# Kernel optimization log

Hardware: AMD Instinct MI355X
Metric: run time of the kernel (lower is better)

Reference implementation:

```python
import jax, jax.numpy as jnp
import numpy as np


def _sage_conv(x, src, dst, num_nodes, Wl, Wr, b):
    # PyG SAGEConv (aggr='mean'): out = lin_l(mean_{j in N(i)} x_j) + lin_r(x_i)
    msgs = x[src]                                            # [E, d] gather
    agg = jax.ops.segment_sum(msgs, dst, num_segments=num_nodes)   # [N, d]
    deg = jax.ops.segment_sum(jnp.ones((src.shape[0],), x.dtype), dst,
                              num_segments=num_nodes)        # [N]
    mean = agg / jnp.clip(deg, 1.0)[:, None]                 # isolated nodes -> 0
    return mean @ Wl.T + b + x @ Wr.T


def setup_inputs() -> dict:
    key = jax.random.key(0)
    ks = jax.random.split(key, 12)
    N, E, d = 100000, 1600000, 64
    sizes = [64, 64, 32]
    x = jax.random.normal(ks[0], (N, d), dtype=jnp.float32)
    edge_index = jax.random.randint(ks[1], (2, E), 0, N, dtype=jnp.int64)
    edge_weight = jax.random.uniform(ks[2], (E,), dtype=jnp.float32)
    inp = {"x": x, "edge_index": edge_index, "edge_weight": edge_weight}
    cur = d
    for i, out_dim in enumerate(sizes):
        s = 1.0 / np.sqrt(cur)
        inp[f"Wl{i}"] = jax.random.uniform(ks[3 + 3 * i], (out_dim, cur), jnp.float32, -s, s)
        inp[f"Wr{i}"] = jax.random.uniform(ks[4 + 3 * i], (out_dim, cur), jnp.float32, -s, s)
        inp[f"b{i}"] = jax.random.uniform(ks[5 + 3 * i], (out_dim,), jnp.float32, -s, s)
        cur = out_dim
    return inp


def reference(x, edge_index, edge_weight, Wl0, Wr0, b0, Wl1, Wr1, b1, Wl2, Wr2, b2):
    # edge_weight is intentionally ignored (GraphSAGE ignores edge weights).
    N = x.shape[0]
    src, dst = edge_index[0], edge_index[1]
    h = jax.nn.relu(_sage_conv(x, src, dst, N, Wl0, Wr0, b0))
    h = jax.nn.relu(_sage_conv(h, src, dst, N, Wl1, Wr1, b1))
    h = _sage_conv(h, src, dst, N, Wl2, Wr2, b2)
    return h
```

## Files before the change

kernel.cpp:

```cpp
#include <hip/hip_runtime.h>
#include <hip/hip_fp16.h>


#define MAXB 512
#define NBLK 512
#define NSLICE 8

typedef _Float16 f16;
typedef __attribute__((ext_vector_type(4))) _Float16 f16x4;
typedef __attribute__((ext_vector_type(8))) _Float16 f16x8;
typedef __attribute__((ext_vector_type(4))) float f32x4;

__global__ __launch_bounds__(256) void hist_k(const int* __restrict__ dst, int E,
                                              int nb, int* __restrict__ ghist) {
    __shared__ int h[MAXB];
    for (int i = threadIdx.x; i < nb; i += 256) h[i] = 0;
    __syncthreads();
    int chunk = (E + NBLK - 1) / NBLK;
    int e0 = blockIdx.x * chunk, e1 = min(e0 + chunk, E);
    for (int e = e0 + threadIdx.x; e < e1; e += 256) atomicAdd(&h[dst[e] >> 8], 1);
    __syncthreads();
    for (int i = threadIdx.x; i < nb; i += 256) ghist[blockIdx.x * MAXB + i] = h[i];
}

__global__ __launch_bounds__(512) void col_scan_k(int* __restrict__ ghist,
                                                  int* __restrict__ colsum) {
    int bucket = blockIdx.x;
    int t = threadIdx.x;
    __shared__ int s[NBLK];
    int v = ghist[t * MAXB + bucket];
    s[t] = v;
    __syncthreads();
    for (int off = 1; off < NBLK; off <<= 1) {
        int x = (t >= off) ? s[t - off] : 0;
        __syncthreads();
        s[t] += x;
        __syncthreads();
    }
    ghist[t * MAXB + bucket] = s[t] - v;
    if (t == NBLK - 1) colsum[bucket] = s[NBLK - 1];
}

__global__ __launch_bounds__(512) void bucket_scan_k(const int* __restrict__ colsum,
                                                     int* __restrict__ bbase, int nb) {
    __shared__ int s[512];
    int t = threadIdx.x;
    int v = (t < nb) ? colsum[t] : 0;
    s[t] = v;
    __syncthreads();
    for (int off = 1; off < 512; off <<= 1) {
        int x = (t >= off) ? s[t - off] : 0;
        __syncthreads();
        s[t] += x;
        __syncthreads();
    }
    if (t < nb) bbase[t] = s[t] - v;
}

__global__ __launch_bounds__(256) void partition_k(const int* __restrict__ src,
                                                   const int* __restrict__ dst,
                                                   const int* __restrict__ ghist,
                                                   const int* __restrict__ bbase,
                                                   unsigned* __restrict__ pairs,
                                                   int E, int nb) {
    __shared__ int cur[MAXB];
    for (int i = threadIdx.x; i < nb; i += 256)
        cur[i] = bbase[i] + ghist[blockIdx.x * MAXB + i];
    __syncthreads();
    int chunk = (E + NBLK - 1) / NBLK;
    int e0 = blockIdx.x * chunk, e1 = min(e0 + chunk, E);
    for (int e = e0 + threadIdx.x; e < e1; e += 256) {
        int d = dst[e];
        int b = d >> 8;
        int pos = atomicAdd(&cur[b], 1);
        pairs[pos] = ((unsigned)(d & 255) << 24) | (unsigned)src[e];
    }
}

__global__ __launch_bounds__(256) void bucket_fill2_k(const unsigned* __restrict__ pairs,
                                                      const int* __restrict__ bbase,
                                                      const int* __restrict__ colsum,
                                                      int* __restrict__ rowptr,
                                                      int* __restrict__ adj,
                                                      int N, int E) {
    int b = blockIdx.x, t = threadIdx.x;
    int node0 = b << 8;
    int nloc = min(256, N - node0);
    int e0 = bbase[b];
    int e1 = e0 + colsum[b];
    __shared__ int cnt[256 * NSLICE];
    __shared__ int base[256 * NSLICE];
    __shared__ int bs[256];
#pragma unroll
    for (int k = 0; k < NSLICE; k++) cnt[t * NSLICE + k] = 0;
    __syncthreads();
    for (int e = e0 + t; e < e1; e += 256) {
        unsigned p = pairs[e];
        int local = p >> 24;
        int s = (int)((p & 0xFFFFFFu) >> 14);
        atomicAdd(&cnt[local * NSLICE + s], 1);
    }
    __syncthreads();
    int lv[NSLICE];
    int lsum = 0;
#pragma unroll
    for (int k = 0; k < NSLICE; k++) { lv[k] = cnt[t * NSLICE + k]; lsum += lv[k]; }
    bs[t] = lsum;
    __syncthreads();
    for (int off = 1; off < 256; off <<= 1) {
        int x = (t >= off) ? bs[t - off] : 0;
        __syncthreads();
        bs[t] += x;
        __syncthreads();
    }
    int run = e0 + bs[t] - lsum;
    if (t < nloc) rowptr[node0 + t] = run;
    if (b == 0 && t == 0) rowptr[N] = E;
#pragma unroll
    for (int k = 0; k < NSLICE; k++) { base[t * NSLICE + k] = run; run += lv[k]; }
#pragma unroll
    for (int k = 0; k < NSLICE; k++) cnt[t * NSLICE + k] = 0;
    __syncthreads();
    for (int e = e0 + t; e < e1; e += 256) {
        unsigned p = pairs[e];
        int local = p >> 24;
        int srcv = (int)(p & 0xFFFFFFu);
        int key = local * NSLICE + (srcv >> 14);
        int pos = base[key] + atomicAdd(&cnt[key], 1);
        adj[pos] = srcv;
    }
}


__device__ inline f16x8 cvt2h(float4 a, float4 b) {
    f16x8 o;
    o[0] = (_Float16)a.x; o[1] = (_Float16)a.y; o[2] = (_Float16)a.z; o[3] = (_Float16)a.w;
    o[4] = (_Float16)b.x; o[5] = (_Float16)b.y; o[6] = (_Float16)b.z; o[7] = (_Float16)b.w;
    return o;
}

template <int DOUT, bool AFP32, bool ZF16>
__global__ __launch_bounds__(256) void gemm_mfma_k(const void* __restrict__ A,
                                                   const float* __restrict__ Wl,
                                                   const float* __restrict__ Wr,
                                                   const float* __restrict__ bias,
                                                   __half* __restrict__ Yp,
                                                   void* __restrict__ Zp, int N) {
    constexpr int DOUT2 = 2 * DOUT;
    constexpr int NCT = DOUT2 / 16;
    constexpr int WST = 72;
    __shared__ f16 wlds[DOUT2 * WST];
    int t = threadIdx.x;

    for (int i = t; i < DOUT2 * 16; i += 256) {
        int col = i >> 4, j4 = i & 15;
        const float* wsrc = (col < DOUT) ? (Wl + (size_t)col * 64)
                                         : (Wr + (size_t)(col - DOUT) * 64);
        float4 w = *reinterpret_cast<const float4*>(wsrc + j4 * 4);
        f16x4 o;
        o[0] = (_Float16)w.x; o[1] = (_Float16)w.y;
        o[2] = (_Float16)w.z; o[3] = (_Float16)w.w;
        *reinterpret_cast<f16x4*>(&wlds[col * WST + j4 * 4]) = o;
    }
    __syncthreads();

    int lane = t & 63, wv = t >> 6;
    int r16 = lane & 15;
    int kg = lane >> 4;

    f16x8 bf[NCT][2];
#pragma unroll
    for (int ct = 0; ct < NCT; ct++)
#pragma unroll
        for (int kt = 0; kt < 2; kt++)
            bf[ct][kt] = *reinterpret_cast<const f16x8*>(
                &wlds[(ct * 16 + r16) * WST + kt * 32 + kg * 8]);

    float4 bias4[NCT / 2];
#pragma unroll
    for (int ct = NCT / 2; ct < NCT; ct++)
        bias4[ct - NCT / 2] =
            *reinterpret_cast<const float4*>(bias + ct * 16 + kg * 4 - DOUT);

    int rbase = blockIdx.x * 256 + wv * 64;

#pragma unroll
    for (int rt = 0; rt < 4; rt++) {
        int row0 = rbase + rt * 16;
        int arow = row0 + r16;
        bool valid = arow < N;
        int ar = valid ? arow : (N - 1);

        f16x8 af[2];
        if (AFP32) {
            const float* Af = reinterpret_cast<const float*>(A) + (size_t)ar * 64;
#pragma unroll
            for (int kt = 0; kt < 2; kt++) {
                float4 u = *reinterpret_cast<const float4*>(Af + kt * 32 + kg * 8);
                float4 v = *reinterpret_cast<const float4*>(Af + kt * 32 + kg * 8 + 4);
                af[kt] = cvt2h(u, v);
            }
        } else {
            const f16* Ah = reinterpret_cast<const f16*>(A) + (size_t)ar * 64;
            af[0] = *reinterpret_cast<const f16x8*>(Ah + kg * 8);
            af[1] = *reinterpret_cast<const f16x8*>(Ah + 32 + kg * 8);
        }

        f32x4 acc[NCT];
#pragma unroll
        for (int ct = 0; ct < NCT; ct++) acc[ct] = (f32x4){0.f, 0.f, 0.f, 0.f};
#pragma unroll
        for (int kt = 0; kt < 2; kt++)
#pragma unroll
            for (int ct = 0; ct < NCT; ct++)
                acc[ct] = __builtin_amdgcn_mfma_f32_16x16x32_f16(
                    bf[ct][kt], af[kt], acc[ct], 0, 0, 0);

        if (valid) {
#pragma unroll
            for (int ct = 0; ct < NCT; ct++) {
                int c0 = ct * 16 + kg * 4;
                if (c0 < DOUT) {
                    f16x4 o;
                    o[0] = (_Float16)acc[ct][0]; o[1] = (_Float16)acc[ct][1];
                    o[2] = (_Float16)acc[ct][2]; o[3] = (_Float16)acc[ct][3];
                    *reinterpret_cast<f16x4*>(
                        reinterpret_cast<f16*>(Yp) + (size_t)arow * DOUT + c0) = o;
                } else {
                    float4 bv = bias4[ct - NCT / 2];
                    if (ZF16) {
                        f16x4 z;
                        z[0] = (_Float16)(acc[ct][0] + bv.x);
                        z[1] = (_Float16)(acc[ct][1] + bv.y);
                        z[2] = (_Float16)(acc[ct][2] + bv.z);
                        z[3] = (_Float16)(acc[ct][3] + bv.w);
                        *reinterpret_cast<f16x4*>(
                            reinterpret_cast<f16*>(Zp) + (size_t)arow * DOUT + (c0 - DOUT)) = z;
                    } else {
                        float4 z;
                        z.x = acc[ct][0] + bv.x; z.y = acc[ct][1] + bv.y;
                        z.z = acc[ct][2] + bv.z; z.w = acc[ct][3] + bv.w;
                        *reinterpret_cast<float4*>(
                            reinterpret_cast<float*>(Zp) + (size_t)arow * DOUT + (c0 - DOUT)) = z;
                    }
                }
            }
        }
    }
}


template <int DOUT, bool RELU, bool OUTF16>
__global__ __launch_bounds__(256) void aggregate_k(const int* __restrict__ rp,
                                                   const int* __restrict__ adj,
                                                   const __half* __restrict__ Yh,
                                                   const __half* __restrict__ Zh,
                                                   __half* __restrict__ Ho,
                                                   float* __restrict__ Hf, int N) {
    constexpr int FPR = DOUT / 8;
    constexpr int NPW = 64 / FPR;
    int wave = threadIdx.x >> 6;
    int lane = threadIdx.x & 63;
    int g = lane / FPR;
    int d8 = lane % FPR;
    int node = (blockIdx.x * 4 + wave) * NPW + g;
    if (node >= N) return;
    int s0 = rp[node], s1 = rp[node + 1];
    const float4* Y4 = reinterpret_cast<const float4*>(Yh);
    float acc[8];
#pragma unroll
    for (int k = 0; k < 8; k++) acc[k] = 0.f;

    int e = s0;
    for (; e + 4 <= s1; e += 4) {
        int a0 = adj[e], a1 = adj[e + 1], a2 = adj[e + 2], a3 = adj[e + 3];
        float4 r0 = Y4[(unsigned)a0 * FPR + d8];
        float4 r1 = Y4[(unsigned)a1 * FPR + d8];
        float4 r2 = Y4[(unsigned)a2 * FPR + d8];
        float4 r3 = Y4[(unsigned)a3 * FPR + d8];
        const __half2* h0 = reinterpret_cast<const __half2*>(&r0);
        const __half2* h1 = reinterpret_cast<const __half2*>(&r1);
        const __half2* h2 = reinterpret_cast<const __half2*>(&r2);
        const __half2* h3 = reinterpret_cast<const __half2*>(&r3);
#pragma unroll
        for (int k = 0; k < 4; k++) {
            float2 f0 = __half22float2(h0[k]);
            float2 f1 = __half22float2(h1[k]);
            float2 f2 = __half22float2(h2[k]);
            float2 f3 = __half22float2(h3[k]);
            acc[2 * k]     += (f0.x + f1.x) + (f2.x + f3.x);
            acc[2 * k + 1] += (f0.y + f1.y) + (f2.y + f3.y);
        }
    }
    for (; e < s1; e++) {
        float4 r0 = Y4[(unsigned)adj[e] * FPR + d8];
        const __half2* h0 = reinterpret_cast<const __half2*>(&r0);
#pragma unroll
        for (int k = 0; k < 4; k++) {
            float2 f0 = __half22float2(h0[k]);
            acc[2 * k] += f0.x;
            acc[2 * k + 1] += f0.y;
        }
    }
    int deg = s1 - s0;
    float inv = (deg > 0) ? 1.f / (float)deg : 0.f;

    if constexpr (OUTF16) {
        f16x8 zf = *reinterpret_cast<const f16x8*>(
            reinterpret_cast<const f16*>(Zh) + (size_t)node * DOUT + d8 * 8);
        f16x8 o;
#pragma unroll
        for (int k = 0; k < 8; k++) {
            float tv = (float)zf[k] + acc[k] * inv;
            if (RELU) tv = fmaxf(tv, 0.f);
            o[k] = (_Float16)tv;
        }
        *reinterpret_cast<f16x8*>(reinterpret_cast<f16*>(Ho) + (size_t)node * DOUT + d8 * 8) = o;
    } else {
        float4* H4 = reinterpret_cast<float4*>(Hf);
        size_t hb = (size_t)node * (DOUT / 4) + d8 * 2;
        float4 v0 = H4[hb], v1 = H4[hb + 1];
        v0.x += acc[0] * inv; v0.y += acc[1] * inv;
        v0.z += acc[2] * inv; v0.w += acc[3] * inv;
        v1.x += acc[4] * inv; v1.y += acc[5] * inv;
        v1.z += acc[6] * inv; v1.w += acc[7] * inv;
        if (RELU) {
            v0.x = fmaxf(v0.x, 0.f); v0.y = fmaxf(v0.y, 0.f);
            v0.z = fmaxf(v0.z, 0.f); v0.w = fmaxf(v0.w, 0.f);
            v1.x = fmaxf(v1.x, 0.f); v1.y = fmaxf(v1.y, 0.f);
            v1.z = fmaxf(v1.z, 0.f); v1.w = fmaxf(v1.w, 0.f);
        }
        H4[hb] = v0;
        H4[hb + 1] = v1;
    }
}


extern "C" void kernel_launch(void* const* d_in, const int* in_sizes, int n_in,
                              void* d_out, int out_size, void* d_ws, size_t ws_size,
                              hipStream_t stream) {
    const float* x = (const float*)d_in[0];
    const int* ei = (const int*)d_in[1];
    const float* Wl0 = (const float*)d_in[3];
    const float* Wr0 = (const float*)d_in[4];
    const float* b0 = (const float*)d_in[5];
    const float* Wl1 = (const float*)d_in[6];
    const float* Wr1 = (const float*)d_in[7];
    const float* b1 = (const float*)d_in[8];
    const float* Wl2 = (const float*)d_in[9];
    const float* Wr2 = (const float*)d_in[10];
    const float* b2 = (const float*)d_in[11];

    int N = in_sizes[0] / 64;
    int E = in_sizes[1] / 2;
    const int* src = ei;
    const int* dstp = ei + E;

    char* ws = (char*)d_ws;
    size_t off = 0;
    auto take = [&](size_t bytes) -> void* {
        void* p = ws + off;
        off = (off + bytes + 255) & ~(size_t)255;
        return p;
    };
    int* rowptr = (int*)take((size_t)(N + 1) * 4);
    int* ghist = (int*)take((size_t)NBLK * MAXB * 4);
    int* colsum = (int*)take(MAXB * 4);
    int* bbase = (int*)take(MAXB * 4);
    int* adj = (int*)take((size_t)E * 4);
    __half* Yh = (__half*)take((size_t)N * 64 * 2);
    __half* Zbuf = (__half*)take((size_t)N * 64 * 2);
    __half* HA = (__half*)take((size_t)N * 64 * 2);
    __half* HB = (__half*)take((size_t)N * 64 * 2);
    (void)ws_size;
    (void)n_in;
    (void)out_size;

    unsigned* pairs = (unsigned*)Yh;

    int nb = (N + 255) / 256;

    hist_k<<<NBLK, 256, 0, stream>>>(dstp, E, nb, ghist);
    col_scan_k<<<nb, 512, 0, stream>>>(ghist, colsum);
    bucket_scan_k<<<1, 512, 0, stream>>>(colsum, bbase, nb);
    partition_k<<<NBLK, 256, 0, stream>>>(src, dstp, ghist, bbase, pairs, E, nb);
    bucket_fill2_k<<<nb, 256, 0, stream>>>(pairs, bbase, colsum, rowptr, adj, N, E);

    float* out = (float*)d_out;
    int gb = (N + 255) / 256;
    int ab64 = (N + 31) / 32;
    int ab32 = (N + 63) / 64;

    gemm_mfma_k<64, true, true><<<gb, 256, 0, stream>>>(x, Wl0, Wr0, b0, Yh, Zbuf, N);
    aggregate_k<64, true, true><<<ab64, 256, 0, stream>>>(rowptr, adj, Yh, Zbuf, HA, nullptr, N);
    gemm_mfma_k<64, false, true><<<gb, 256, 0, stream>>>(HA, Wl1, Wr1, b1, Yh, Zbuf, N);
    aggregate_k<64, true, true><<<ab64, 256, 0, stream>>>(rowptr, adj, Yh, Zbuf, HB, nullptr, N);
    gemm_mfma_k<32, false, false><<<gb, 256, 0, stream>>>(HB, Wl2, Wr2, b2, Yh, out, N);
    aggregate_k<32, false, false><<<ab32, 256, 0, stream>>>(rowptr, adj, Yh, nullptr, nullptr, out, N);
}
```

Before: 168.2 us.

## Fuse neighbor aggregation with next layer's MFMA GEMM via LDS staging

```diff
diff --git a/kernel.cpp b/kernel.cpp
--- a/kernel.cpp
+++ b/kernel.cpp
@@ -138,6 +138,7 @@
     o[4] = (_Float16)b.x; o[5] = (_Float16)b.y; o[6] = (_Float16)b.z; o[7] = (_Float16)b.w;
     return o;
 }
+
 
 template <int DOUT, bool AFP32, bool ZF16>
 __global__ __launch_bounds__(256) void gemm_mfma_k(const void* __restrict__ A,
@@ -250,12 +251,173 @@
 }
 
 
-template <int DOUT, bool RELU, bool OUTF16>
+template <int DOUT, bool ZF16OUT>
+__global__ __launch_bounds__(256) void fused_agg_gemm_k(const int* __restrict__ rp,
+                                                        const int* __restrict__ adj,
+                                                        const __half* __restrict__ Yin,
+                                                        const __half* __restrict__ Zin,
+                                                        const float* __restrict__ Wl,
+                                                        const float* __restrict__ Wr,
+                                                        const float* __restrict__ bias,
+                                                        __half* __restrict__ Yp,
+                                                        void* __restrict__ Zp, int N) {
+    constexpr int DOUT2 = 2 * DOUT;
+    constexpr int NCT = DOUT2 / 16;
+    constexpr int WST = 72;
+    constexpr int HST = 80;
+    __shared__ f16 wlds[DOUT2 * WST];
+    __shared__ f16 hlds[128 * HST];
+    int t = threadIdx.x;
+
+    for (int i = t; i < DOUT2 * 16; i += 256) {
+        int col = i >> 4, j4 = i & 15;
+        const float* wsrc = (col < DOUT) ? (Wl + (size_t)col * 64)
+                                         : (Wr + (size_t)(col - DOUT) * 64);
+        float4 w = *reinterpret_cast<const float4*>(wsrc + j4 * 4);
+        f16x4 o;
+        o[0] = (_Float16)w.x; o[1] = (_Float16)w.y;
+        o[2] = (_Float16)w.z; o[3] = (_Float16)w.w;
+        *reinterpret_cast<f16x4*>(&wlds[col * WST + j4 * 4]) = o;
+    }
+
+    int lane = t & 63, wv = t >> 6;
+
+    {
+        int g = lane >> 3;
+        int d8 = lane & 7;
+        const float4* Y4 = reinterpret_cast<const float4*>(Yin);
+#pragma unroll
+        for (int pass = 0; pass < 4; ++pass) {
+            int nl = wv * 32 + pass * 8 + g;
+            int node = blockIdx.x * 128 + nl;
+            if (node < N) {
+                int s0 = rp[node], s1 = rp[node + 1];
+                float acc[8];
+#pragma unroll
+                for (int k = 0; k < 8; k++) acc[k] = 0.f;
+                int e = s0;
+                for (; e + 4 <= s1; e += 4) {
+                    int a0 = adj[e], a1 = adj[e + 1], a2 = adj[e + 2], a3 = adj[e + 3];
+                    float4 r0 = Y4[(unsigned)a0 * 8 + d8];
+                    float4 r1 = Y4[(unsigned)a1 * 8 + d8];
+                    float4 r2 = Y4[(unsigned)a2 * 8 + d8];
+                    float4 r3 = Y4[(unsigned)a3 * 8 + d8];
+                    const __half2* h0 = reinterpret_cast<const __half2*>(&r0);
+                    const __half2* h1 = reinterpret_cast<const __half2*>(&r1);
+                    const __half2* h2 = reinterpret_cast<const __half2*>(&r2);
+                    const __half2* h3 = reinterpret_cast<const __half2*>(&r3);
+#pragma unroll
+                    for (int k = 0; k < 4; k++) {
+                        float2 f0 = __half22float2(h0[k]);
+                        float2 f1 = __half22float2(h1[k]);
+                        float2 f2 = __half22float2(h2[k]);
+                        float2 f3 = __half22float2(h3[k]);
+                        acc[2 * k]     += (f0.x + f1.x) + (f2.x + f3.x);
+                        acc[2 * k + 1] += (f0.y + f1.y) + (f2.y + f3.y);
+                    }
+                }
+                for (; e < s1; e++) {
+                    float4 r0 = Y4[(unsigned)adj[e] * 8 + d8];
+                    const __half2* h0 = reinterpret_cast<const __half2*>(&r0);
+#pragma unroll
+                    for (int k = 0; k < 4; k++) {
+                        float2 f0 = __half22float2(h0[k]);
+                        acc[2 * k] += f0.x;
+                        acc[2 * k + 1] += f0.y;
+                    }
+                }
+                int deg = s1 - s0;
+                float inv = (deg > 0) ? 1.f / (float)deg : 0.f;
+                f16x8 zf = *reinterpret_cast<const f16x8*>(
+                    reinterpret_cast<const f16*>(Zin) + (size_t)node * 64 + d8 * 8);
+                f16x8 o;
+#pragma unroll
+                for (int k = 0; k < 8; k++) {
+                    float tv = (float)zf[k] + acc[k] * inv;
+                    tv = fmaxf(tv, 0.f);
+                    o[k] = (_Float16)tv;
+                }
+                *reinterpret_cast<f16x8*>(&hlds[nl * HST + d8 * 8]) = o;
+            }
+        }
+    }
+    __syncthreads();
+
+    int r16 = lane & 15;
+    int kg = lane >> 4;
+
+    f16x8 bf[NCT][2];
+#pragma unroll
+    for (int ct = 0; ct < NCT; ct++)
+#pragma unroll
+        for (int kt = 0; kt < 2; kt++)
+            bf[ct][kt] = *reinterpret_cast<const f16x8*>(
+                &wlds[(ct * 16 + r16) * WST + kt * 32 + kg * 8]);
+
+    float4 bias4[NCT / 2];
+#pragma unroll
+    for (int ct = NCT / 2; ct < NCT; ct++)
+        bias4[ct - NCT / 2] =
+            *reinterpret_cast<const float4*>(bias + ct * 16 + kg * 4 - DOUT);
+
+#pragma unroll
+    for (int rt = 0; rt < 2; rt++) {
+        int rl = wv * 32 + rt * 16 + r16;
+        int arow = blockIdx.x * 128 + rl;
+        bool valid = arow < N;
+
+        f16x8 af[2];
+        af[0] = *reinterpret_cast<const f16x8*>(&hlds[rl * HST + kg * 8]);
+        af[1] = *reinterpret_cast<const f16x8*>(&hlds[rl * HST + 32 + kg * 8]);
+
+        f32x4 acc[NCT];
+#pragma unroll
+        for (int ct = 0; ct < NCT; ct++) acc[ct] = (f32x4){0.f, 0.f, 0.f, 0.f};
+#pragma unroll
+        for (int kt = 0; kt < 2; kt++)
+#pragma unroll
+            for (int ct = 0; ct < NCT; ct++)
+                acc[ct] = __builtin_amdgcn_mfma_f32_16x16x32_f16(
+                    bf[ct][kt], af[kt], acc[ct], 0, 0, 0);
+
+        if (valid) {
+#pragma unroll
+            for (int ct = 0; ct < NCT; ct++) {
+                int c0 = ct * 16 + kg * 4;
+                if (c0 < DOUT) {
+                    f16x4 o;
+                    o[0] = (_Float16)acc[ct][0]; o[1] = (_Float16)acc[ct][1];
+                    o[2] = (_Float16)acc[ct][2]; o[3] = (_Float16)acc[ct][3];
+                    *reinterpret_cast<f16x4*>(
+                        reinterpret_cast<f16*>(Yp) + (size_t)arow * DOUT + c0) = o;
+                } else {
+                    float4 bv = bias4[ct - NCT / 2];
+                    if (ZF16OUT) {
+                        f16x4 z;
+                        z[0] = (_Float16)(acc[ct][0] + bv.x);
+                        z[1] = (_Float16)(acc[ct][1] + bv.y);
+                        z[2] = (_Float16)(acc[ct][2] + bv.z);
+                        z[3] = (_Float16)(acc[ct][3] + bv.w);
+                        *reinterpret_cast<f16x4*>(
+                            reinterpret_cast<f16*>(Zp) + (size_t)arow * DOUT + (c0 - DOUT)) = z;
+                    } else {
+                        float4 z;
+                        z.x = acc[ct][0] + bv.x; z.y = acc[ct][1] + bv.y;
+                        z.z = acc[ct][2] + bv.z; z.w = acc[ct][3] + bv.w;
+                        *reinterpret_cast<float4*>(
+                            reinterpret_cast<float*>(Zp) + (size_t)arow * DOUT + (c0 - DOUT)) = z;
+                    }
+                }
+            }
+        }
+    }
+}
+
+
+template <int DOUT, bool RELU>
 __global__ __launch_bounds__(256) void aggregate_k(const int* __restrict__ rp,
                                                    const int* __restrict__ adj,
                                                    const __half* __restrict__ Yh,
-                                                   const __half* __restrict__ Zh,
-                                                   __half* __restrict__ Ho,
                                                    float* __restrict__ Hf, int N) {
     constexpr int FPR = DOUT / 8;
     constexpr int NPW = 64 / FPR;
@@ -304,35 +466,21 @@
     }
     int deg = s1 - s0;
     float inv = (deg > 0) ? 1.f / (float)deg : 0.f;
-
-    if constexpr (OUTF16) {
-        f16x8 zf = *reinterpret_cast<const f16x8*>(
-            reinterpret_cast<const f16*>(Zh) + (size_t)node * DOUT + d8 * 8);
-        f16x8 o;
-#pragma unroll
-        for (int k = 0; k < 8; k++) {
-            float tv = (float)zf[k] + acc[k] * inv;
-            if (RELU) tv = fmaxf(tv, 0.f);
-            o[k] = (_Float16)tv;
-        }
-        *reinterpret_cast<f16x8*>(reinterpret_cast<f16*>(Ho) + (size_t)node * DOUT + d8 * 8) = o;
-    } else {
-        float4* H4 = reinterpret_cast<float4*>(Hf);
-        size_t hb = (size_t)node * (DOUT / 4) + d8 * 2;
-        float4 v0 = H4[hb], v1 = H4[hb + 1];
-        v0.x += acc[0] * inv; v0.y += acc[1] * inv;
-        v0.z += acc[2] * inv; v0.w += acc[3] * inv;
-        v1.x += acc[4] * inv; v1.y += acc[5] * inv;
-        v1.z += acc[6] * inv; v1.w += acc[7] * inv;
-        if (RELU) {
-            v0.x = fmaxf(v0.x, 0.f); v0.y = fmaxf(v0.y, 0.f);
-            v0.z = fmaxf(v0.z, 0.f); v0.w = fmaxf(v0.w, 0.f);
-            v1.x = fmaxf(v1.x, 0.f); v1.y = fmaxf(v1.y, 0.f);
-            v1.z = fmaxf(v1.z, 0.f); v1.w = fmaxf(v1.w, 0.f);
-        }
-        H4[hb] = v0;
-        H4[hb + 1] = v1;
-    }
+    float4* H4 = reinterpret_cast<float4*>(Hf);
+    size_t hb = (size_t)node * (DOUT / 4) + d8 * 2;
+    float4 v0 = H4[hb], v1 = H4[hb + 1];
+    v0.x += acc[0] * inv; v0.y += acc[1] * inv;
+    v0.z += acc[2] * inv; v0.w += acc[3] * inv;
+    v1.x += acc[4] * inv; v1.y += acc[5] * inv;
+    v1.z += acc[6] * inv; v1.w += acc[7] * inv;
+    if (RELU) {
+        v0.x = fmaxf(v0.x, 0.f); v0.y = fmaxf(v0.y, 0.f);
+        v0.z = fmaxf(v0.z, 0.f); v0.w = fmaxf(v0.w, 0.f);
+        v1.x = fmaxf(v1.x, 0.f); v1.y = fmaxf(v1.y, 0.f);
+        v1.z = fmaxf(v1.z, 0.f); v1.w = fmaxf(v1.w, 0.f);
+    }
+    H4[hb] = v0;
+    H4[hb + 1] = v1;
 }
 
 
@@ -368,15 +516,14 @@
     int* colsum = (int*)take(MAXB * 4);
     int* bbase = (int*)take(MAXB * 4);
     int* adj = (int*)take((size_t)E * 4);
-    __half* Yh = (__half*)take((size_t)N * 64 * 2);
+    __half* Ya = (__half*)take((size_t)N * 64 * 2);
+    __half* Yb = (__half*)take((size_t)N * 64 * 2);
     __half* Zbuf = (__half*)take((size_t)N * 64 * 2);
-    __half* HA = (__half*)take((size_t)N * 64 * 2);
-    __half* HB = (__half*)take((size_t)N * 64 * 2);
     (void)ws_size;
     (void)n_in;
     (void)out_size;
 
-    unsigned* pairs = (unsigned*)Yh;
+    unsigned* pairs = (unsigned*)Ya;
 
     int nb = (N + 255) / 256;
 
@@ -388,13 +535,13 @@
 
     float* out = (float*)d_out;
     int gb = (N + 255) / 256;
-    int ab64 = (N + 31) / 32;
+    int fb = (N + 127) / 128;
     int ab32 = (N + 63) / 64;
 
-    gemm_mfma_k<64, true, true><<<gb, 256, 0, stream>>>(x, Wl0, Wr0, b0, Yh, Zbuf, N);
-    aggregate_k<64, true, true><<<ab64, 256, 0, stream>>>(rowptr, adj, Yh, Zbuf, HA, nullptr, N);
-    gemm_mfma_k<64, false, true><<<gb, 256, 0, stream>>>(HA, Wl1, Wr1, b1, Yh, Zbuf, N);
-    aggregate_k<64, true, true><<<ab64, 256, 0, stream>>>(rowptr, adj, Yh, Zbuf, HB, nullptr, N);
-    gemm_mfma_k<32, false, false><<<gb, 256, 0, stream>>>(HB, Wl2, Wr2, b2, Yh, out, N);
-    aggregate_k<32, false, false><<<ab32, 256, 0, stream>>>(rowptr, adj, Yh, nullptr, nullptr, out, N);
-}
+    gemm_mfma_k<64, true, true><<<gb, 256, 0, stream>>>(x, Wl0, Wr0, b0, Ya, Zbuf, N);
+    fused_agg_gemm_k<64, true><<<fb, 256, 0, stream>>>(rowptr, adj, Ya, Zbuf,
+                                                       Wl1, Wr1, b1, Yb, Zbuf, N);
+    fused_agg_gemm_k<32, false><<<fb, 256, 0, stream>>>(rowptr, adj, Yb, Zbuf,
+                                                        Wl2, Wr2, b2, Ya, out, N);
+    aggregate_k<32, false><<<ab32, 256, 0, stream>>>(rowptr, adj, Ya, out, N);
+}
```

New measurement: 193.8 us. 1.15x slower.
